# Optimization experiments

Hardware: AMD Instinct MI355X
Metric: run time of the kernel (lower is better)

## Reference

```python
import jax, jax.numpy as jnp
import numpy as np

N = 50000
E = 1600000
IN_C = 128
HID_C = 128
OUT_C = 64
NUM_REL = 8
NUM_BASES = 4


def rgcn_conv(x, edge_index, edge_type, basis, comp, root, bias):
    """Faithful PyG RGCNConv with basis decomposition and mean aggregation.

    basis: (num_bases, in, out); comp: (num_rel, num_bases);
    root: (in, out); bias: (out,).
    """
    # Compose per-relation weights from bases: W_r = sum_b comp[r,b] * basis[b]
    W = jnp.einsum('rb,bio->rio', comp, basis)  # (R, in, out)
    src, dst = edge_index[0], edge_index[1]
    # Segment id encodes (relation, dst node) so one segment_sum handles all relations
    seg = edge_type * N + dst  # (E,)
    msgs = x[src]  # (E, in) gather
    sums = jax.ops.segment_sum(msgs, seg, num_segments=NUM_REL * N)
    cnt = jax.ops.segment_sum(jnp.ones((seg.shape[0],), dtype=x.dtype), seg,
                              num_segments=NUM_REL * N)
    mean = sums / jnp.maximum(cnt, 1.0)[:, None]  # mean aggr; empty segs -> 0
    agg = mean.reshape(NUM_REL, N, -1)  # (R, N, in)
    out = jnp.einsum('rni,rio->no', agg, W)
    out = out + x @ root + bias  # root/self-loop weight + bias
    return out


def setup_inputs() -> dict:
    key = jax.random.key(0)
    ks = jax.random.split(key, 12)
    x = jax.random.normal(ks[0], (N, IN_C), dtype=jnp.float32)
    A = jax.random.randint(ks[1], (2, E), 0, N, dtype=jnp.int64)
    edge_type = jax.random.randint(ks[2], (E,), 0, NUM_REL, dtype=jnp.int64)
    def glorot(k, shape):
        fan_in, fan_out = shape[-2], shape[-1]
        lim = jnp.sqrt(6.0 / (fan_in + fan_out)).astype(jnp.float32)
        return jax.random.uniform(k, shape, jnp.float32, -lim, lim)
    w1_basis = glorot(ks[3], (NUM_BASES, IN_C, HID_C))
    w1_comp = glorot(ks[4], (NUM_REL, NUM_BASES))
    w1_root = glorot(ks[5], (IN_C, HID_C))
    w1_bias = jnp.zeros((HID_C,), jnp.float32)
    w2_basis = glorot(ks[6], (NUM_BASES, HID_C, OUT_C))
    w2_comp = glorot(ks[7], (NUM_REL, NUM_BASES))
    w2_root = glorot(ks[8], (HID_C, OUT_C))
    w2_bias = jnp.zeros((OUT_C,), jnp.float32)
    return {"x": x, "A": A, "edge_type": edge_type,
            "w1_basis": w1_basis, "w1_comp": w1_comp, "w1_root": w1_root, "w1_bias": w1_bias,
            "w2_basis": w2_basis, "w2_comp": w2_comp, "w2_root": w2_root, "w2_bias": w2_bias}


def reference(x, A, edge_type, w1_basis, w1_comp, w1_root, w1_bias,
              w2_basis, w2_comp, w2_root, w2_bias):
    h = rgcn_conv(x, A, edge_type, w1_basis, w1_comp, w1_root, w1_bias)
    h = jax.nn.relu(h)
    out = rgcn_conv(h, A, edge_type, w2_basis, w2_comp, w2_root, w2_bias)
    return out
```

## Files before the change

### kernel.cpp

```cpp
#include <hip/hip_runtime.h>


#define N_NODES 50000
#define N_EDGES 1600000
#define N_REL   8
#define CAP     32
#define NSEG    (N_REL * N_NODES)

typedef __attribute__((ext_vector_type(8))) short short8;
typedef __attribute__((ext_vector_type(4))) float f32x4;

__device__ __forceinline__ ushort f2bf(float x) {
    unsigned u = __builtin_bit_cast(unsigned, x);
    u += 0x7FFFu + ((u >> 16) & 1u);
    return (ushort)(u >> 16);
}
__device__ __forceinline__ float u2f(unsigned u) {
    return __builtin_bit_cast(float, u);
}

__global__ void zero_i32_kernel(int* __restrict__ p, int n) {
    int i = blockIdx.x * 256 + threadIdx.x;
    if (i < n) p[i] = 0;
}

__global__ void to_bf16_kernel(const float* __restrict__ in,
                               ushort* __restrict__ out,
                               ushort* __restrict__ hbf) {
    int i = blockIdx.x * 256 + threadIdx.x;
    int totx = (N_NODES + 1) * 16;
    if (i < totx) {
        int base = i * 8;
        short8 v;
        if (base < N_NODES * 128) {
            f32x4 a = *(const f32x4*)(in + base);
            f32x4 b = *(const f32x4*)(in + base + 4);
            v = (short8){(short)f2bf(a.x), (short)f2bf(a.y), (short)f2bf(a.z),
                         (short)f2bf(a.w), (short)f2bf(b.x), (short)f2bf(b.y),
                         (short)f2bf(b.z), (short)f2bf(b.w)};
        } else {
            v = (short8){0, 0, 0, 0, 0, 0, 0, 0};
        }
        *(short8*)(out + base) = v;
    } else if (i < totx + 16) {
        int idx = i - totx;
        *(short8*)(hbf + (size_t)N_NODES * 128 + idx * 8) =
            (short8){0, 0, 0, 0, 0, 0, 0, 0};
    }
}

__global__ void compose_wt_kernel(const float* __restrict__ basis1,
                                  const float* __restrict__ comp1,
                                  const float* __restrict__ root1,
                                  const float* __restrict__ basis2,
                                  const float* __restrict__ comp2,
                                  const float* __restrict__ root2,
                                  ushort* __restrict__ Wt1,
                                  ushort* __restrict__ Wt2) {
    constexpr int T1 = 9 * 128 * 128;
    constexpr int T2 = 9 * 64 * 128;
    int i = blockIdx.x * 256 + threadIdx.x;
    if (i >= T1 + T2) return;
    const float* basis;
    const float* comp;
    const float* root;
    ushort* Wt;
    int outc, ii;
    if (i < T1) {
        basis = basis1; comp = comp1; root = root1; Wt = Wt1;
        outc = 128; ii = i;
    } else {
        basis = basis2; comp = comp2; root = root2; Wt = Wt2;
        outc = 64; ii = i - T1;
    }
    int per_r = outc << 7;
    int r = ii / per_r;
    int rem = ii - r * per_r;
    int n = rem >> 7;
    int k = rem & 127;
    float s;
    if (r == N_REL) {
        s = root[k * outc + n];
    } else {
        s = 0.f;
#pragma unroll
        for (int b = 0; b < 4; ++b)
            s += comp[r * 4 + b] * basis[(b * 128 + k) * outc + n];
    }
    Wt[ii] = f2bf(s);
}

__global__ void build_ell_kernel(const int* __restrict__ A,
                                 const int* __restrict__ etype,
                                 int* __restrict__ cnt,
                                 ushort* __restrict__ ell) {
    int e = blockIdx.x * 256 + threadIdx.x;
    if (e >= N_EDGES) return;
    int s = __builtin_nontemporal_load(A + e);
    int d = __builtin_nontemporal_load(A + N_EDGES + e);
    int t = __builtin_nontemporal_load(etype + e);
    int seg = t * N_NODES + d;
    int slot = atomicAdd(&cnt[seg], 1);
    if (slot < CAP) ell[(size_t)seg * CAP + slot] = (ushort)s;
}

template <int OUTC, bool RELU, bool BF16OUT>
__global__ __launch_bounds__(512, 8)
void rgcn_layer_mfma(const ushort* __restrict__ xbf,
                     const int* __restrict__ cnt,
                     const ushort* __restrict__ ell,
                     const ushort* __restrict__ Wt,
                     const float* __restrict__ bias,
                     void* __restrict__ outp) {
    constexpr int LDK = 136;
    constexpr int TN  = 64;
    constexpr int NCH = OUTC / 32;

    __shared__ ushort meanT[TN * LDK];
    __shared__ ushort Wl[32 * LDK];

    const int tid   = threadIdx.x;
    const int lane  = tid & 63;
    const int wave  = tid >> 6;
    const int nbase = blockIdx.x * TN;

    const int g  = tid >> 4;
    const int j  = tid & 15;
    const int j8 = j * 8;
    const int gb = lane & 48;

    const int rt = wave & 3;
    const int ch = wave >> 2;
    const int lr = lane & 15;
    const int kc = (lane >> 4) * 8;

    f32x4 acc[NCH];
#pragma unroll
    for (int t = 0; t < NCH; ++t) acc[t] = (f32x4){0.f, 0.f, 0.f, 0.f};

    for (int r = 0; r <= N_REL; ++r) {
#pragma unroll
        for (int p = 0; p < 2; ++p) {
            int a  = p * 32 + g;
            int gn = nbase + a;
            short8 sv = (short8){0, 0, 0, 0, 0, 0, 0, 0};
            if (gn < N_NODES) {
                if (r == N_REL) {
                    sv = *(const short8*)(xbf + (size_t)gn * 128 + j8);
                } else {
                    int seg = r * N_NODES + gn;
                    int c   = cnt[seg];
                    int cc  = c < CAP ? c : CAP;
                    uint pre = *(const uint*)(ell + (size_t)seg * CAP + 2 * j);
                    f32x4 s0 = (f32x4){0.f, 0.f, 0.f, 0.f};
                    f32x4 s1 = (f32x4){0.f, 0.f, 0.f, 0.f};
                    int ccr = (cc + 3) & ~3;
                    for (int e = 0; e < ccr; e += 4) {
                        uint ua = __shfl(pre, gb + (e >> 1), 64);
                        uint ub = __shfl(pre, gb + (e >> 1) + 1, 64);
                        int i0 = (e + 0 < cc) ? (int)(ua & 0xFFFFu) : N_NODES;
                        int i1 = (e + 1 < cc) ? (int)(ua >> 16)     : N_NODES;
                        int i2 = (e + 2 < cc) ? (int)(ub & 0xFFFFu) : N_NODES;
                        int i3 = (e + 3 < cc) ? (int)(ub >> 16)     : N_NODES;
                        short8 v0 = *(const short8*)(xbf + (size_t)i0 * 128 + j8);
                        short8 v1 = *(const short8*)(xbf + (size_t)i1 * 128 + j8);
                        short8 v2 = *(const short8*)(xbf + (size_t)i2 * 128 + j8);
                        short8 v3 = *(const short8*)(xbf + (size_t)i3 * 128 + j8);
#pragma unroll
                        for (int u = 0; u < 4; ++u) {
                            short8 v = (u == 0) ? v0 : (u == 1) ? v1
                                     : (u == 2) ? v2 : v3;
                            uint4 w = __builtin_bit_cast(uint4, v);
                            s0.x += u2f(w.x << 16);
                            s0.y += u2f(w.x & 0xFFFF0000u);
                            s0.z += u2f(w.y << 16);
                            s0.w += u2f(w.y & 0xFFFF0000u);
                            s1.x += u2f(w.z << 16);
                            s1.y += u2f(w.z & 0xFFFF0000u);
                            s1.z += u2f(w.w << 16);
                            s1.w += u2f(w.w & 0xFFFF0000u);
                        }
                    }
                    float inv = 1.f / (float)(c > 1 ? c : 1);
                    s0 *= inv;
                    s1 *= inv;
                    sv = (short8){(short)f2bf(s0.x), (short)f2bf(s0.y),
                                  (short)f2bf(s0.z), (short)f2bf(s0.w),
                                  (short)f2bf(s1.x), (short)f2bf(s1.y),
                                  (short)f2bf(s1.z), (short)f2bf(s1.w)};
                }
            }
            *(short8*)&meanT[a * LDK + j8] = sv;
        }
        __syncthreads();

        short8 af[4];
        const int m = rt * 16 + lr;
#pragma unroll
        for (int ks = 0; ks < 4; ++ks)
            af[ks] = *(const short8*)&meanT[m * LDK + ks * 32 + kc];

#pragma unroll
        for (int c = 0; c < NCH; ++c) {
            {
                const float4* src =
                    (const float4*)(Wt + ((size_t)r * OUTC + c * 32) * 128);
                int n  = tid >> 4;
                int k8 = tid & 15;
                *(float4*)&Wl[n * LDK + k8 * 8] = src[tid];
            }
            __syncthreads();
            const int n = ch * 16 + lr;
            f32x4 a = acc[c];
#pragma unroll
            for (int ks = 0; ks < 4; ++ks) {
                short8 bf = *(const short8*)&Wl[n * LDK + ks * 32 + kc];
                a = __builtin_amdgcn_mfma_f32_16x16x32_bf16(af[ks], bf, a,
                                                            0, 0, 0);
            }
            acc[c] = a;
            if (c + 1 < NCH) __syncthreads();
        }
    }

    const int rq = (lane >> 4) * 4;
#pragma unroll
    for (int t = 0; t < NCH; ++t) {
        int col  = t * 32 + ch * 16 + lr;
        float bv = bias[col];
#pragma unroll
        for (int q = 0; q < 4; ++q) {
            int node = nbase + rt * 16 + rq + q;
            if (node < N_NODES) {
                float v = acc[t][q] + bv;
                if (RELU) v = fmaxf(v, 0.f);
                if (BF16OUT)
                    __builtin_nontemporal_store(
                        f2bf(v), (ushort*)outp + (size_t)node * OUTC + col);
                else
                    __builtin_nontemporal_store(
                        v, (float*)outp + (size_t)node * OUTC + col);
            }
        }
    }
}

extern "C" void kernel_launch(void* const* d_in, const int* in_sizes, int n_in,
                              void* d_out, int out_size, void* d_ws, size_t ws_size,
                              hipStream_t stream) {
    const float* x        = (const float*)d_in[0];
    const int*   A        = (const int*)d_in[1];
    const int*   etype    = (const int*)d_in[2];
    const float* w1_basis = (const float*)d_in[3];
    const float* w1_comp  = (const float*)d_in[4];
    const float* w1_root  = (const float*)d_in[5];
    const float* w1_bias  = (const float*)d_in[6];
    const float* w2_basis = (const float*)d_in[7];
    const float* w2_comp  = (const float*)d_in[8];
    const float* w2_root  = (const float*)d_in[9];
    const float* w2_bias  = (const float*)d_in[10];
    float* out = (float*)d_out;

    char* ws = (char*)d_ws;
    ushort* Wt1  = (ushort*)(ws);
    ushort* Wt2  = (ushort*)(ws + (512 << 10));
    int*    cnt  = (int*)(ws + (1 << 20));
    ushort* x_bf = (ushort*)(ws + (3ull << 20));
    ushort* h_bf = (ushort*)(ws + (16ull << 20));
    ushort* ell  = (ushort*)(ws + (29ull << 20));

    zero_i32_kernel<<<(NSEG + 255) / 256, 256, 0, stream>>>(cnt, NSEG);
    to_bf16_kernel<<<((N_NODES + 1) * 16 + 16 + 255) / 256, 256, 0, stream>>>(
        x, x_bf, h_bf);
    compose_wt_kernel<<<(9 * 128 * 128 + 9 * 64 * 128 + 255) / 256, 256, 0,
                      stream>>>(w1_basis, w1_comp, w1_root,
                                w2_basis, w2_comp, w2_root, Wt1, Wt2);
    build_ell_kernel<<<(N_EDGES + 255) / 256, 256, 0, stream>>>(A, etype, cnt, ell);

    int grid = (N_NODES + 63) / 64;
    rgcn_layer_mfma<128, true, true><<<grid, 512, 0, stream>>>(
        x_bf, cnt, ell, Wt1, w1_bias, h_bf);
    rgcn_layer_mfma<64, false, false><<<grid, 512, 0, stream>>>(
        h_bf, cnt, ell, Wt2, w2_bias, out);
}
```

Before: 368.8 us.

## Merge prep kernels, halve layer tile, prefetch next relation's ELL metadata

```diff
diff --git a/kernel.cpp b/kernel.cpp
--- a/kernel.cpp
+++ b/kernel.cpp
@@ -7,6 +7,10 @@
 #define CAP     32
 #define NSEG    (N_REL * N_NODES)
 
+#define NB_BUILD 6250
+#define NB_X     3126
+#define NB_W     864
+
 typedef __attribute__((ext_vector_type(8))) short short8;
 typedef __attribute__((ext_vector_type(4))) float f32x4;
 
@@ -24,88 +28,91 @@
     if (i < n) p[i] = 0;
 }
 
-__global__ void to_bf16_kernel(const float* __restrict__ in,
-                               ushort* __restrict__ out,
-                               ushort* __restrict__ hbf) {
-    int i = blockIdx.x * 256 + threadIdx.x;
-    int totx = (N_NODES + 1) * 16;
-    if (i < totx) {
-        int base = i * 8;
-        short8 v;
-        if (base < N_NODES * 128) {
-            f32x4 a = *(const f32x4*)(in + base);
-            f32x4 b = *(const f32x4*)(in + base + 4);
-            v = (short8){(short)f2bf(a.x), (short)f2bf(a.y), (short)f2bf(a.z),
-                         (short)f2bf(a.w), (short)f2bf(b.x), (short)f2bf(b.y),
-                         (short)f2bf(b.z), (short)f2bf(b.w)};
-        } else {
-            v = (short8){0, 0, 0, 0, 0, 0, 0, 0};
-        }
-        *(short8*)(out + base) = v;
-    } else if (i < totx + 16) {
-        int idx = i - totx;
-        *(short8*)(hbf + (size_t)N_NODES * 128 + idx * 8) =
-            (short8){0, 0, 0, 0, 0, 0, 0, 0};
-    }
-}
-
-__global__ void compose_wt_kernel(const float* __restrict__ basis1,
-                                  const float* __restrict__ comp1,
-                                  const float* __restrict__ root1,
-                                  const float* __restrict__ basis2,
-                                  const float* __restrict__ comp2,
-                                  const float* __restrict__ root2,
-                                  ushort* __restrict__ Wt1,
-                                  ushort* __restrict__ Wt2) {
-    constexpr int T1 = 9 * 128 * 128;
-    constexpr int T2 = 9 * 64 * 128;
-    int i = blockIdx.x * 256 + threadIdx.x;
-    if (i >= T1 + T2) return;
-    const float* basis;
-    const float* comp;
-    const float* root;
-    ushort* Wt;
-    int outc, ii;
-    if (i < T1) {
-        basis = basis1; comp = comp1; root = root1; Wt = Wt1;
-        outc = 128; ii = i;
-    } else {
-        basis = basis2; comp = comp2; root = root2; Wt = Wt2;
-        outc = 64; ii = i - T1;
-    }
-    int per_r = outc << 7;
-    int r = ii / per_r;
-    int rem = ii - r * per_r;
-    int n = rem >> 7;
-    int k = rem & 127;
-    float s;
-    if (r == N_REL) {
-        s = root[k * outc + n];
-    } else {
-        s = 0.f;
-#pragma unroll
-        for (int b = 0; b < 4; ++b)
-            s += comp[r * 4 + b] * basis[(b * 128 + k) * outc + n];
-    }
-    Wt[ii] = f2bf(s);
-}
-
-__global__ void build_ell_kernel(const int* __restrict__ A,
+__global__ void mega_prep_kernel(const int* __restrict__ A,
                                  const int* __restrict__ etype,
                                  int* __restrict__ cnt,
-                                 ushort* __restrict__ ell) {
-    int e = blockIdx.x * 256 + threadIdx.x;
-    if (e >= N_EDGES) return;
-    int s = __builtin_nontemporal_load(A + e);
-    int d = __builtin_nontemporal_load(A + N_EDGES + e);
-    int t = __builtin_nontemporal_load(etype + e);
-    int seg = t * N_NODES + d;
-    int slot = atomicAdd(&cnt[seg], 1);
-    if (slot < CAP) ell[(size_t)seg * CAP + slot] = (ushort)s;
+                                 ushort* __restrict__ ell,
+                                 const float* __restrict__ x,
+                                 ushort* __restrict__ xbf,
+                                 ushort* __restrict__ hbf,
+                                 const float* __restrict__ basis1,
+                                 const float* __restrict__ comp1,
+                                 const float* __restrict__ root1,
+                                 const float* __restrict__ basis2,
+                                 const float* __restrict__ comp2,
+                                 const float* __restrict__ root2,
+                                 ushort* __restrict__ Wt1,
+                                 ushort* __restrict__ Wt2) {
+    const int bid = blockIdx.x;
+    const int tid = threadIdx.x;
+    if (bid < NB_BUILD) {
+        int e = bid * 256 + tid;
+        if (e < N_EDGES) {
+            int s = __builtin_nontemporal_load(A + e);
+            int d = __builtin_nontemporal_load(A + N_EDGES + e);
+            int t = __builtin_nontemporal_load(etype + e);
+            int seg = t * N_NODES + d;
+            int slot = atomicAdd(&cnt[seg], 1);
+            if (slot < CAP) ell[(size_t)seg * CAP + slot] = (ushort)s;
+        }
+    } else if (bid < NB_BUILD + NB_X) {
+        int i = (bid - NB_BUILD) * 256 + tid;
+        int totx = (N_NODES + 1) * 16;
+        if (i < totx) {
+            int base = i * 8;
+            short8 v;
+            if (base < N_NODES * 128) {
+                f32x4 a = *(const f32x4*)(x + base);
+                f32x4 b = *(const f32x4*)(x + base + 4);
+                v = (short8){(short)f2bf(a.x), (short)f2bf(a.y), (short)f2bf(a.z),
+                             (short)f2bf(a.w), (short)f2bf(b.x), (short)f2bf(b.y),
+                             (short)f2bf(b.z), (short)f2bf(b.w)};
+            } else {
+                v = (short8){0, 0, 0, 0, 0, 0, 0, 0};
+            }
+            *(short8*)(xbf + base) = v;
+        } else if (i < totx + 16) {
+            int idx = i - totx;
+            *(short8*)(hbf + (size_t)N_NODES * 128 + idx * 8) =
+                (short8){0, 0, 0, 0, 0, 0, 0, 0};
+        }
+    } else {
+        constexpr int T1 = 9 * 128 * 128;
+        constexpr int T2 = 9 * 64 * 128;
+        int i = (bid - NB_BUILD - NB_X) * 256 + tid;
+        if (i >= T1 + T2) return;
+        const float* basis;
+        const float* comp;
+        const float* root;
+        ushort* Wt;
+        int outc, ii;
+        if (i < T1) {
+            basis = basis1; comp = comp1; root = root1; Wt = Wt1;
+            outc = 128; ii = i;
+        } else {
+            basis = basis2; comp = comp2; root = root2; Wt = Wt2;
+            outc = 64; ii = i - T1;
+        }
+        int per_r = outc << 7;
+        int r = ii / per_r;
+        int rem = ii - r * per_r;
+        int n = rem >> 7;
+        int k = rem & 127;
+        float s;
+        if (r == N_REL) {
+            s = root[k * outc + n];
+        } else {
+            s = 0.f;
+#pragma unroll
+            for (int b = 0; b < 4; ++b)
+                s += comp[r * 4 + b] * basis[(b * 128 + k) * outc + n];
+        }
+        Wt[ii] = f2bf(s);
+    }
 }
 
 template <int OUTC, bool RELU, bool BF16OUT>
-__global__ __launch_bounds__(512, 8)
+__global__ __launch_bounds__(256, 8)
 void rgcn_layer_mfma(const ushort* __restrict__ xbf,
                      const int* __restrict__ cnt,
                      const ushort* __restrict__ ell,
@@ -113,7 +120,7 @@
                      const float* __restrict__ bias,
                      void* __restrict__ outp) {
     constexpr int LDK = 136;
-    constexpr int TN  = 64;
+    constexpr int TN  = 32;
     constexpr int NCH = OUTC / 32;
 
     __shared__ ushort meanT[TN * LDK];
@@ -129,11 +136,21 @@
     const int j8 = j * 8;
     const int gb = lane & 48;
 
-    const int rt = wave & 3;
-    const int ch = wave >> 2;
+    const int rt = wave & 1;
+    const int ch = wave >> 1;
     const int lr = lane & 15;
     const int kc = (lane >> 4) * 8;
 
+    const int gn0 = nbase + g;
+    const int gn1 = nbase + 16 + g;
+    const int sg0 = gn0 < N_NODES ? gn0 : 0;
+    const int sg1 = gn1 < N_NODES ? gn1 : 0;
+
+    int  pc0 = cnt[sg0];
+    int  pc1 = cnt[sg1];
+    uint pe0 = *(const uint*)(ell + (size_t)sg0 * CAP + 2 * j);
+    uint pe1 = *(const uint*)(ell + (size_t)sg1 * CAP + 2 * j);
+
     f32x4 acc[NCH];
 #pragma unroll
     for (int t = 0; t < NCH; ++t) acc[t] = (f32x4){0.f, 0.f, 0.f, 0.f};
@@ -141,17 +158,16 @@
     for (int r = 0; r <= N_REL; ++r) {
 #pragma unroll
         for (int p = 0; p < 2; ++p) {
-            int a  = p * 32 + g;
-            int gn = nbase + a;
+            int gn = p ? gn1 : gn0;
+            int a  = p * 16 + g;
             short8 sv = (short8){0, 0, 0, 0, 0, 0, 0, 0};
             if (gn < N_NODES) {
                 if (r == N_REL) {
                     sv = *(const short8*)(xbf + (size_t)gn * 128 + j8);
                 } else {
-                    int seg = r * N_NODES + gn;
-                    int c   = cnt[seg];
-                    int cc  = c < CAP ? c : CAP;
-                    uint pre = *(const uint*)(ell + (size_t)seg * CAP + 2 * j);
+                    int  c   = p ? pc1 : pc0;
+                    uint pre = p ? pe1 : pe0;
+                    int  cc  = c < CAP ? c : CAP;
                     f32x4 s0 = (f32x4){0.f, 0.f, 0.f, 0.f};
                     f32x4 s1 = (f32x4){0.f, 0.f, 0.f, 0.f};
                     int ccr = (cc + 3) & ~3;
@@ -192,6 +208,14 @@
             }
             *(short8*)&meanT[a * LDK + j8] = sv;
         }
+
+        if (r + 1 < N_REL) {
+            size_t so = (size_t)(r + 1) * N_NODES;
+            pc0 = cnt[so + sg0];
+            pc1 = cnt[so + sg1];
+            pe0 = *(const uint*)(ell + (so + sg0) * CAP + 2 * j);
+            pe1 = *(const uint*)(ell + (so + sg1) * CAP + 2 * j);
+        }
         __syncthreads();
 
         short8 af[4];
@@ -205,9 +229,13 @@
             {
                 const float4* src =
                     (const float4*)(Wt + ((size_t)r * OUTC + c * 32) * 128);
-                int n  = tid >> 4;
-                int k8 = tid & 15;
-                *(float4*)&Wl[n * LDK + k8 * 8] = src[tid];
+#pragma unroll
+                for (int q = 0; q < 2; ++q) {
+                    int idx = tid + q * 256;
+                    int n   = idx >> 4;
+                    int k8  = idx & 15;
+                    *(float4*)&Wl[n * LDK + k8 * 8] = src[idx];
+                }
             }
             __syncthreads();
             const int n = ch * 16 + lr;
@@ -270,16 +298,13 @@
     ushort* ell  = (ushort*)(ws + (29ull << 20));
 
     zero_i32_kernel<<<(NSEG + 255) / 256, 256, 0, stream>>>(cnt, NSEG);
-    to_bf16_kernel<<<((N_NODES + 1) * 16 + 16 + 255) / 256, 256, 0, stream>>>(
-        x, x_bf, h_bf);
-    compose_wt_kernel<<<(9 * 128 * 128 + 9 * 64 * 128 + 255) / 256, 256, 0,
-                      stream>>>(w1_basis, w1_comp, w1_root,
-                                w2_basis, w2_comp, w2_root, Wt1, Wt2);
-    build_ell_kernel<<<(N_EDGES + 255) / 256, 256, 0, stream>>>(A, etype, cnt, ell);
-
-    int grid = (N_NODES + 63) / 64;
-    rgcn_layer_mfma<128, true, true><<<grid, 512, 0, stream>>>(
+    mega_prep_kernel<<<NB_BUILD + NB_X + NB_W, 256, 0, stream>>>(
+        A, etype, cnt, ell, x, x_bf, h_bf,
+        w1_basis, w1_comp, w1_root, w2_basis, w2_comp, w2_root, Wt1, Wt2);
+
+    int grid = (N_NODES + 31) / 32;
+    rgcn_layer_mfma<128, true, true><<<grid, 256, 0, stream>>>(
         x_bf, cnt, ell, Wt1, w1_bias, h_bf);
-    rgcn_layer_mfma<64, false, false><<<grid, 512, 0, stream>>>(
+    rgcn_layer_mfma<64, false, false><<<grid, 256, 0, stream>>>(
         h_bf, cnt, ell, Wt2, w2_bias, out);
 }
```

After: 360.5 us. 1.02x faster.
